# Kernel tuning notes

Measured on AMD Instinct MI355X. Metric: run time of the kernel, lower is better.

The kernel has to match this reference:

```python
import jax, jax.numpy as jnp
import numpy as np
import math

DIM = 896
NH = 8
HD = DIM // NH  # 112
B, T, KA_RAW, KT = 64, 8, 64, 512
KA = KA_RAW + 1  # adapter tokens + p conditioning token


def rope_cos_sin(L, hd):
    inv = 1.0 / (10000.0 ** (jnp.arange(0, hd, 2, dtype=jnp.float32) / hd))
    freqs = jnp.arange(L, dtype=jnp.float32)[:, None] * inv[None, :]  # (L, hd/2)
    emb = jnp.concatenate([freqs, freqs], axis=-1)  # (L, hd)
    return jnp.cos(emb), jnp.sin(emb)


def rotate_half(x):
    # interleaved rotation, faithful to the torch code
    x1 = x[..., ::2]
    x2 = x[..., 1::2]
    return jnp.stack((-x2, x1), axis=-1).reshape(x.shape)


def rope_apply(t, cos, sin):
    # cos/sin: (L, hd) broadcast over (B, H, L, hd)
    return t * cos + rotate_half(t) * sin


def heads(t):
    Bb, L, _ = t.shape
    return t.reshape(Bb, L, NH, HD).transpose(0, 2, 1, 3)  # (B, H, L, hd)


def setup_inputs() -> dict:
    key = jax.random.key(0)
    ks = jax.random.split(key, 32)
    s = 0.02
    d = {
        'x': jax.random.normal(ks[0], (B, T, DIM), jnp.float32),
        'h_a': jax.random.normal(ks[1], (B, KA_RAW, DIM), jnp.float32),
        'h_t': jax.random.normal(ks[2], (B, KT, DIM), jnp.float32),
        'p': jax.random.normal(ks[3], (B, 1, DIM), jnp.float32),
    }
    names = ['Wq', 'Wks', 'Wvs', 'Wka', 'Wva', 'Wkt', 'Wvt', 'Wo', 'Wf']
    for i, n in enumerate(names):
        d[n] = s * jax.random.normal(ks[4 + i], (DIM, DIM), jnp.float32)
        d['b' + n[1:]] = s * jax.random.normal(ks[16 + i], (DIM,), jnp.float32)
    d['gate'] = jnp.full((1,), 0.1, jnp.float32)  # nonzero so task branch is active
    d['ln_g'] = jnp.ones((DIM,), jnp.float32)
    d['ln_b'] = jnp.zeros((DIM,), jnp.float32)
    return d


def reference(x, h_a, h_t, p,
              Wq, bq, Wks, bks, Wvs, bvs, Wka, bka, Wva, bva,
              Wkt, bkt, Wvt, bvt, Wo, bo, Wf, bf,
              gate, ln_g, ln_b):
    ratio_g = jnp.tanh(gate)  # (1,)
    h_ad = jnp.concatenate([h_a, p], axis=1)  # (B, KA, C)

    q = heads(x @ Wq + bq)            # (B,H,T,hd)
    k_s = heads(x @ Wks + bks)
    v_s = heads(x @ Wvs + bvs)
    k_a = heads(h_ad @ Wka + bka)     # (B,H,KA,hd)
    v_a = heads(h_ad @ Wva + bva)
    k_t = heads(h_t @ Wkt + bkt)      # (B,H,KT,hd)
    v_t = heads(h_t @ Wvt + bvt)

    cos_m, sin_m = rope_cos_sin(T, HD)
    q = rope_apply(q, cos_m, sin_m)
    k_s = rope_apply(k_s, cos_m, sin_m)
    cos_a, sin_a = rope_cos_sin(KA, HD)
    k_a = rope_apply(k_a, cos_a, sin_a)
    cos_t, sin_t = rope_cos_sin(KT, HD)
    k_t = rope_apply(k_t, cos_t, sin_t)

    s_self = jnp.einsum('bhtd,bhkd->bhtk', q, k_s)
    s_ad = jnp.einsum('bhtd,bhkd->bhtk', q, k_a)
    s_task = jnp.einsum('bhtd,bhkd->bhtk', q, k_t) * ratio_g
    scores = jnp.concatenate([s_self, s_ad, s_task], axis=-1) / math.sqrt(HD)
    w = jax.nn.softmax(scores, axis=-1)  # (B,H,T,T+KA+KT)

    v = jnp.concatenate([v_s, v_a, v_t], axis=2)  # (B,H,T+KA+KT,hd)
    out = jnp.einsum('bhtk,bhkd->bhtd', w, v)
    out = out.transpose(0, 2, 1, 3).reshape(x.shape)  # (B,T,C)
    out = out @ Wo + bo

    y = out + x
    mu = jnp.mean(y, axis=-1, keepdims=True)
    var = jnp.var(y, axis=-1, keepdims=True)
    yn = (y - mu) / jnp.sqrt(var + 1e-5) * ln_g + ln_b
    return jax.nn.relu(yn @ Wf + bf)
```

## Files before the change

kernel.cpp:

```cpp
#include <hip/hip_runtime.h>
#include <hip/hip_bf16.h>
#include <math.h>

#define DIM 896
#define DD  (DIM * DIM)
#define NH 8
#define HD 112
#define BB 64
#define TT 8
#define KA 65
#define KAPAD 4224
#define KT 512
#define NKEYS (TT + KA + KT)
#define CH 4096

#define EPI_NONE  0
#define EPI_ROPE  1
#define EPI_RESID 2
#define EPI_RELU  3

#define NEG_L2_10K_OVER_56 (-0.2373327285062406f)

#ifndef __has_builtin
#define __has_builtin(x) 0
#endif
#if __has_builtin(__builtin_amdgcn_global_load_lds)
#define HAS_GLL 1
#else
#define HAS_GLL 0
#endif

typedef __attribute__((ext_vector_type(8))) short bf16x8_t;
typedef __attribute__((ext_vector_type(4))) float f32x4_t;

__device__ __forceinline__ short f2bf(float f) {
  unsigned u = __float_as_uint(f);
  u += 0x7fffu + ((u >> 16) & 1u);
  return (short)(u >> 16);
}
__device__ __forceinline__ float bf2f(short s) {
  return __uint_as_float(((unsigned)(unsigned short)s) << 16);
}

struct W9 { const float* w[9]; };

__global__ __launch_bounds__(256) void wtrans(W9 ws, short* __restrict__ Wt)
{
  __shared__ float t[32][33];
  const float* W = ws.w[blockIdx.z];
  short* dst = Wt + (size_t)blockIdx.z * DD;
  const int bx = blockIdx.x, by = blockIdx.y;
  const int tx = threadIdx.x & 31, ty = threadIdx.x >> 5;
#pragma unroll
  for (int i = 0; i < 4; ++i)
    t[ty + i * 8][tx] = W[(size_t)(by * 32 + ty + i * 8) * DIM + bx * 32 + tx];
  __syncthreads();
#pragma unroll
  for (int i = 0; i < 4; ++i)
    dst[(size_t)(bx * 32 + ty + i * 8) * DIM + by * 32 + tx] = f2bf(t[tx][ty + i * 8]);
}

__global__ __launch_bounds__(256) void convert_bf16(
    const float* __restrict__ src, short* __restrict__ dst, int n8)
{
  const int i = blockIdx.x * 256 + threadIdx.x;
  if (i >= n8) return;
  const float4 a = ((const float4*)src)[i * 2];
  const float4 b = ((const float4*)src)[i * 2 + 1];
  bf16x8_t o;
  o[0] = f2bf(a.x); o[1] = f2bf(a.y); o[2] = f2bf(a.z); o[3] = f2bf(a.w);
  o[4] = f2bf(b.x); o[5] = f2bf(b.y); o[6] = f2bf(b.z); o[7] = f2bf(b.w);
  ((bf16x8_t*)dst)[i] = o;
}

__global__ __launch_bounds__(256) void build_had(
    const float* __restrict__ h_a, const float* __restrict__ p,
    short* __restrict__ had)
{
  const int i = blockIdx.x * 256 + threadIdx.x;
  const int total = KAPAD * DIM / 8;
  if (i >= total) return;
  const int c = (i % 112) * 8;
  const int row = i / 112;
  bf16x8_t o;
  if (row >= BB * KA) {
#pragma unroll
    for (int j = 0; j < 8; ++j) o[j] = 0;
  } else {
    const int b = row / KA, j = row % KA;
    const float* src = (j < KA - 1) ? h_a + ((size_t)b * (KA - 1) + j) * DIM + c
                                    : p + (size_t)b * DIM + c;
    const float4 a = *(const float4*)src;
    const float4 d = *(const float4*)(src + 4);
    o[0] = f2bf(a.x); o[1] = f2bf(a.y); o[2] = f2bf(a.z); o[3] = f2bf(a.w);
    o[4] = f2bf(d.x); o[5] = f2bf(d.y); o[6] = f2bf(d.z); o[7] = f2bf(d.w);
  }
  ((bf16x8_t*)had)[i] = o;
}

struct EpiCfg {
  const float* bias[3];
  float* outF[3];
  short* outB[3];
  const float* resid;
  int epi[3];
  int pos_mod[3];
  int row_off;
  int hm[3];
  int hm_L[3];
  int hm_ltot[3];
};

__global__ __launch_bounds__(256) void gemm_bf16(
    const short* __restrict__ A, const short* __restrict__ Wt, EpiCfg cfg)
{
  __shared__ __align__(16) short As[128 * 32];
  __shared__ __align__(16) short Bs[128 * 32];
  const int tid = threadIdx.x;
  const int wave = tid >> 6, lane = tid & 63;
  const int sub = blockIdx.x / 7;
  const int col0 = (blockIdx.x % 7) * 128;
  const int row0 = blockIdx.y * 128;
  const int wm = wave >> 1, wn = wave & 1;
  const int lm = lane & 15, lq = lane >> 4;

  const int sm = lane >> 2, sk = (lane & 3) * 8;
  const short* Ag0 = A + (size_t)(row0 + wave * 32 + sm) * DIM + sk;
  const short* Ag1 = Ag0 + (size_t)16 * DIM;
  const short* Wg0 = Wt + (size_t)(sub * DIM + col0 + wave * 32 + sm) * DIM + sk;
  const short* Wg1 = Wg0 + (size_t)16 * DIM;

  f32x4_t acc[4][4];
#pragma unroll
  for (int i = 0; i < 4; ++i)
#pragma unroll
    for (int j = 0; j < 4; ++j) acc[i][j] = (f32x4_t){0.f, 0.f, 0.f, 0.f};

  for (int k0 = 0; k0 < DIM; k0 += 32) {
    __syncthreads();
#if HAS_GLL
    __builtin_amdgcn_global_load_lds(
        (const __attribute__((address_space(1))) unsigned*)(Ag0 + k0),
        (__attribute__((address_space(3))) unsigned*)&As[(wave * 32) * 32], 16, 0, 0);
    __builtin_amdgcn_global_load_lds(
        (const __attribute__((address_space(1))) unsigned*)(Ag1 + k0),
        (__attribute__((address_space(3))) unsigned*)&As[(wave * 32 + 16) * 32], 16, 0, 0);
    __builtin_amdgcn_global_load_lds(
        (const __attribute__((address_space(1))) unsigned*)(Wg0 + k0),
        (__attribute__((address_space(3))) unsigned*)&Bs[(wave * 32) * 32], 16, 0, 0);
    __builtin_amdgcn_global_load_lds(
        (const __attribute__((address_space(1))) unsigned*)(Wg1 + k0),
        (__attribute__((address_space(3))) unsigned*)&Bs[(wave * 32 + 16) * 32], 16, 0, 0);
#else
    {
      const int m = tid >> 1, kh = (tid & 1) * 16;
      *(bf16x8_t*)&As[m * 32 + kh] =
          *(const bf16x8_t*)(A + (size_t)(row0 + m) * DIM + k0 + kh);
      *(bf16x8_t*)&As[m * 32 + kh + 8] =
          *(const bf16x8_t*)(A + (size_t)(row0 + m) * DIM + k0 + kh + 8);
      *(bf16x8_t*)&Bs[m * 32 + kh] =
          *(const bf16x8_t*)(Wt + (size_t)(sub * DIM + col0 + m) * DIM + k0 + kh);
      *(bf16x8_t*)&Bs[m * 32 + kh + 8] =
          *(const bf16x8_t*)(Wt + (size_t)(sub * DIM + col0 + m) * DIM + k0 + kh + 8);
    }
#endif
    __syncthreads();

    bf16x8_t af[4], bfr[4];
#pragma unroll
    for (int t = 0; t < 4; ++t)
      af[t] = *(const bf16x8_t*)&As[(wm * 64 + t * 16 + lm) * 32 + lq * 8];
#pragma unroll
    for (int t = 0; t < 4; ++t)
      bfr[t] = *(const bf16x8_t*)&Bs[(wn * 64 + t * 16 + lm) * 32 + lq * 8];
#pragma unroll
    for (int tm = 0; tm < 4; ++tm)
#pragma unroll
      for (int tn = 0; tn < 4; ++tn)
        acc[tm][tn] = __builtin_amdgcn_mfma_f32_16x16x32_bf16(
            af[tm], bfr[tn], acc[tm][tn], 0, 0, 0);
  }

  const float* bias = cfg.bias[sub];
  float* outF = cfg.outF[sub];
  short* outB = cfg.outB[sub];
  const int epi = cfg.epi[sub], pm = cfg.pos_mod[sub];
  const int hm = cfg.hm[sub];
  const int L = cfg.hm_L[sub], ltot = cfg.hm_ltot[sub];
  int gb[4][4], gl[4][4];
  if (hm) {
#pragma unroll
    for (int tm = 0; tm < 4; ++tm) {
      const int g = cfg.row_off + row0 + wm * 64 + tm * 16 + lq * 4;
      int bq2 = g / L;
      int l = g - bq2 * L;
#pragma unroll
      for (int r = 0; r < 4; ++r) {
        gb[tm][r] = bq2; gl[tm][r] = l;
        if (++l == L) { l = 0; ++bq2; }
      }
    }
  }
#pragma unroll
  for (int tn = 0; tn < 4; ++tn) {
    const int col = col0 + wn * 64 + tn * 16 + lm;
    const float bv = bias[col];
    int hcol = 0, dcol = 0;
    if (hm) { hcol = col / HD; dcol = col - hcol * HD; }
    float fr = 0.f, sgn = 0.f;
    if (epi == EPI_ROPE) {
      const int d0 = col % HD;
      fr = exp2f((float)(d0 % 56) * NEG_L2_10K_OVER_56);
      sgn = (d0 & 1) ? 1.f : -1.f;
    }
#pragma unroll
    for (int tm = 0; tm < 4; ++tm) {
#pragma unroll
      for (int r = 0; r < 4; ++r) {
        const int grow = cfg.row_off + row0 + wm * 64 + tm * 16 + lq * 4 + r;
        float v = acc[tm][tn][r] + bv;
        if (epi == EPI_ROPE) {
          const float prt = __shfl_xor(v, 1);
          const int pos = hm ? gl[tm][r] : (grow % pm);
          float s, c;
          __sincosf((float)pos * fr, &s, &c);
          v = v * c + sgn * prt * s;
        } else if (epi == EPI_RESID) {
          v += cfg.resid[(size_t)grow * DIM + col];
        } else if (epi == EPI_RELU) {
          v = fmaxf(v, 0.f);
        }
        if (hm) {
          if (gb[tm][r] < BB)
            outB[((size_t)(gb[tm][r] * NH + hcol) * ltot + gl[tm][r]) * HD + dcol] =
                f2bf(v);
        } else if (outB) {
          outB[(size_t)grow * DIM + col] = f2bf(v);
        } else {
          outF[(size_t)grow * DIM + col] = v;
        }
      }
    }
  }
}

#define SCP 10

__global__ __launch_bounds__(1024, 8) void attn_kernel(
    const short* __restrict__ q, const short* __restrict__ kall,
    const short* __restrict__ vall, const float* __restrict__ gate,
    short* __restrict__ out)
{
  __shared__ __align__(16) float qs[TT * HD];
  __shared__ __align__(16) float sc[NKEYS * SCP];
  __shared__ float red[TT * TT * HD];
  __shared__ float isum[TT];
  const int tid = threadIdx.x;
  const int bh = blockIdx.x;
  const float scale = 0.09449111825230681f;
  const float rg = tanhf(gate[0]);

  if (tid < TT * HD) qs[tid] = bf2f(q[(size_t)bh * (TT * HD) + tid]);
  __syncthreads();

  if (tid < NKEYS) {
    const int k = tid;
    const short* kp = kall + ((size_t)bh * NKEYS + k) * HD;
    float dot[TT] = {};
    for (int d8 = 0; d8 < HD; d8 += 8) {
      const bf16x8_t kv8 = *(const bf16x8_t*)(kp + d8);
      float kf[8];
#pragma unroll
      for (int j = 0; j < 8; ++j) kf[j] = bf2f(kv8[j]);
#pragma unroll
      for (int t = 0; t < TT; ++t) {
        const float4 qa = *(const float4*)&qs[t * HD + d8];
        const float4 qb4 = *(const float4*)&qs[t * HD + d8 + 4];
        dot[t] = fmaf(qa.x, kf[0], dot[t]);
        dot[t] = fmaf(qa.y, kf[1], dot[t]);
        dot[t] = fmaf(qa.z, kf[2], dot[t]);
        dot[t] = fmaf(qa.w, kf[3], dot[t]);
        dot[t] = fmaf(qb4.x, kf[4], dot[t]);
        dot[t] = fmaf(qb4.y, kf[5], dot[t]);
        dot[t] = fmaf(qb4.z, kf[6], dot[t]);
        dot[t] = fmaf(qb4.w, kf[7], dot[t]);
      }
    }
    const float s = (k >= TT + KA) ? scale * rg : scale;
#pragma unroll
    for (int t = 0; t < TT; ++t) sc[k * SCP + t] = dot[t] * s;
  }
  __syncthreads();

  const int wave = tid >> 6, lane = tid & 63;
  if (wave < TT) {
    const int t = wave;
    float m = -1e30f;
    for (int k = lane; k < NKEYS; k += 64) m = fmaxf(m, sc[k * SCP + t]);
#pragma unroll
    for (int o = 32; o >= 1; o >>= 1) m = fmaxf(m, __shfl_xor(m, o));
    float sum = 0.f;
    for (int k = lane; k < NKEYS; k += 64) {
      const float e = expf(sc[k * SCP + t] - m);
      sc[k * SCP + t] = e;
      sum += e;
    }
#pragma unroll
    for (int o = 32; o >= 1; o >>= 1) sum += __shfl_xor(sum, o);
    if (lane == 0) isum[t] = 1.f / sum;
  }
  __syncthreads();

  if (tid < TT * HD) {
    const int g = tid / HD, d = tid - g * HD;
    const int kb = (g * NKEYS) / TT, ke = ((g + 1) * NKEYS) / TT;
    const short* vp = vall + (size_t)bh * (NKEYS * HD) + d;
    float acc[TT] = {};
    for (int k = kb; k < ke; ++k) {
      const float vv = bf2f(vp[(size_t)k * HD]);
      const float2 s0 = *(const float2*)&sc[k * SCP];
      const float2 s1 = *(const float2*)&sc[k * SCP + 2];
      const float2 s2 = *(const float2*)&sc[k * SCP + 4];
      const float2 s3 = *(const float2*)&sc[k * SCP + 6];
      acc[0] = fmaf(s0.x, vv, acc[0]);
      acc[1] = fmaf(s0.y, vv, acc[1]);
      acc[2] = fmaf(s1.x, vv, acc[2]);
      acc[3] = fmaf(s1.y, vv, acc[3]);
      acc[4] = fmaf(s2.x, vv, acc[4]);
      acc[5] = fmaf(s2.y, vv, acc[5]);
      acc[6] = fmaf(s3.x, vv, acc[6]);
      acc[7] = fmaf(s3.y, vv, acc[7]);
    }
#pragma unroll
    for (int t = 0; t < TT; ++t) red[(g * TT + t) * HD + d] = acc[t];
  }
  __syncthreads();

  if (tid < TT * HD) {
    const int t = tid / HD, d = tid - t * HD;
    float a = 0.f;
#pragma unroll
    for (int g = 0; g < TT; ++g) a += red[(g * TT + t) * HD + d];
    out[((size_t)(bh >> 3) * TT + t) * DIM + (bh & 7) * HD + d] = f2bf(a * isum[t]);
  }
}

__global__ __launch_bounds__(256) void ln_kernel(
    const float* __restrict__ y, const float* __restrict__ g,
    const float* __restrict__ beta, short* __restrict__ yn)
{
  __shared__ float s1[4], s2[4];
  const int r = blockIdx.x, tid = threadIdx.x;
  const float* row = y + (size_t)r * DIM;
  float sum = 0.f, sq = 0.f;
  for (int c = tid; c < DIM; c += 256) {
    const float v = row[c];
    sum += v;
    sq = fmaf(v, v, sq);
  }
#pragma unroll
  for (int o = 32; o >= 1; o >>= 1) {
    sum += __shfl_xor(sum, o);
    sq  += __shfl_xor(sq, o);
  }
  const int wave = tid >> 6, lane = tid & 63;
  if (lane == 0) { s1[wave] = sum; s2[wave] = sq; }
  __syncthreads();
  sum = s1[0] + s1[1] + s1[2] + s1[3];
  sq  = s2[0] + s2[1] + s2[2] + s2[3];
  const float mu = sum / DIM;
  const float var = sq / DIM - mu * mu;
  const float rstd = 1.f / sqrtf(var + 1e-5f);
  for (int c = tid; c < DIM; c += 256)
    yn[(size_t)r * DIM + c] = f2bf((row[c] - mu) * rstd * g[c] + beta[c]);
}

extern "C" void kernel_launch(void* const* d_in, const int* in_sizes, int n_in,
                              void* d_out, int out_size, void* d_ws, size_t ws_size,
                              hipStream_t stream)
{
  const float* x   = (const float*)d_in[0];
  const float* h_a = (const float*)d_in[1];
  const float* h_t = (const float*)d_in[2];
  const float* p   = (const float*)d_in[3];
  const float* Wq  = (const float*)d_in[4];  const float* bq  = (const float*)d_in[5];
  const float* Wks = (const float*)d_in[6];  const float* bks = (const float*)d_in[7];
  const float* Wvs = (const float*)d_in[8];  const float* bvs = (const float*)d_in[9];
  const float* Wka = (const float*)d_in[10]; const float* bka = (const float*)d_in[11];
  const float* Wva = (const float*)d_in[12]; const float* bva = (const float*)d_in[13];
  const float* Wkt = (const float*)d_in[14]; const float* bkt = (const float*)d_in[15];
  const float* Wvt = (const float*)d_in[16]; const float* bvt = (const float*)d_in[17];
  const float* Wo  = (const float*)d_in[18]; const float* bo  = (const float*)d_in[19];
  const float* Wf  = (const float*)d_in[20]; const float* bf_ = (const float*)d_in[21];
  const float* gate = (const float*)d_in[22];
  const float* ln_g = (const float*)d_in[23];
  const float* ln_b = (const float*)d_in[24];

  const size_t SZ_HAD = (size_t)KAPAD * DIM * 2;
  const size_t SZ_SM  = (size_t)BB * TT * DIM * 2;
  const size_t SZ_KV  = (size_t)BB * NH * NKEYS * HD * 2;
  const size_t SZ_WT  = (size_t)9 * DD * 2;
  const size_t needed = SZ_HAD + SZ_SM * 4 + SZ_KV * 2 + SZ_WT
                        + (size_t)BB * TT * DIM * 4;
  if (ws_size < needed) return;

  char* wsp = (char*)d_ws;
  short* hadb = (short*)wsp; wsp += SZ_HAD;
  short* xb   = (short*)wsp; wsp += SZ_SM;
  short* qb   = (short*)wsp; wsp += SZ_SM;
  short* kall = (short*)wsp; wsp += SZ_KV;
  short* vall = (short*)wsp; wsp += SZ_KV;
  short* WtA  = (short*)wsp; wsp += SZ_WT;
  short* attn_outb = (short*)wsp; wsp += SZ_SM;
  float* yb   = (float*)wsp; wsp += (size_t)BB * TT * DIM * 4;
  short* ynb  = (short*)wsp; wsp += SZ_SM;
  short* scratch = WtA;

  dim3 blk(256);

  W9 w9; const float* Ws[9] = {Wq, Wks, Wvs, Wka, Wva, Wkt, Wvt, Wo, Wf};
  for (int i = 0; i < 9; ++i) w9.w[i] = Ws[i];
  wtrans<<<dim3(28, 28, 9), blk, 0, stream>>>(w9, WtA);

  convert_bf16<<<(BB * TT * DIM / 8 + 255) / 256, blk, 0, stream>>>(x, xb, BB * TT * DIM / 8);
  build_had<<<(KAPAD * DIM / 8 + 255) / 256, blk, 0, stream>>>(h_a, p, hadb);

  {
    EpiCfg c = {};
    c.bias[0] = bq;  c.outB[0] = qb;   c.epi[0] = EPI_ROPE; c.pos_mod[0] = TT;
    c.hm[0] = 1; c.hm_L[0] = TT; c.hm_ltot[0] = TT;
    c.bias[1] = bks; c.outB[1] = kall; c.epi[1] = EPI_ROPE; c.pos_mod[1] = TT;
    c.hm[1] = 1; c.hm_L[1] = TT; c.hm_ltot[1] = NKEYS;
    c.bias[2] = bvs; c.outB[2] = vall; c.epi[2] = EPI_NONE; c.pos_mod[2] = 1;
    c.hm[2] = 1; c.hm_L[2] = TT; c.hm_ltot[2] = NKEYS;
    gemm_bf16<<<dim3(21, BB * TT / 128), blk, 0, stream>>>(xb, WtA, c);
  }
  {
    EpiCfg c = {};
    c.bias[0] = bka; c.outB[0] = kall + (size_t)TT * HD; c.epi[0] = EPI_ROPE;
    c.pos_mod[0] = KA; c.hm[0] = 1; c.hm_L[0] = KA; c.hm_ltot[0] = NKEYS;
    c.bias[1] = bva; c.outB[1] = vall + (size_t)TT * HD; c.epi[1] = EPI_NONE;
    c.pos_mod[1] = 1; c.hm[1] = 1; c.hm_L[1] = KA; c.hm_ltot[1] = NKEYS;
    gemm_bf16<<<dim3(14, KAPAD / 128), blk, 0, stream>>>(hadb, WtA + (size_t)3 * DD, c);
  }
  for (int m0 = 0; m0 < BB * KT; m0 += CH) {
    convert_bf16<<<(CH * DIM / 8 + 255) / 256, blk, 0, stream>>>(
        h_t + (size_t)m0 * DIM, scratch, CH * DIM / 8);
    EpiCfg c = {};
    c.bias[0] = bkt; c.outB[0] = kall + (size_t)(TT + KA) * HD; c.epi[0] = EPI_ROPE;
    c.pos_mod[0] = KT; c.hm[0] = 1; c.hm_L[0] = KT; c.hm_ltot[0] = NKEYS;
    c.bias[1] = bvt; c.outB[1] = vall + (size_t)(TT + KA) * HD; c.epi[1] = EPI_NONE;
    c.pos_mod[1] = 1; c.hm[1] = 1; c.hm_L[1] = KT; c.hm_ltot[1] = NKEYS;
    c.row_off = m0;
    gemm_bf16<<<dim3(14, CH / 128), blk, 0, stream>>>(scratch, WtA + (size_t)5 * DD, c);
  }

  attn_kernel<<<BB * NH, dim3(1024), 0, stream>>>(qb, kall, vall, gate, attn_outb);

  {
    EpiCfg c = {};
    c.bias[0] = bo; c.outF[0] = yb; c.epi[0] = EPI_RESID; c.pos_mod[0] = 1;
    c.resid = x;
    gemm_bf16<<<dim3(7, BB * TT / 128), blk, 0, stream>>>(attn_outb, WtA + (size_t)7 * DD, c);
  }
  ln_kernel<<<BB * TT, blk, 0, stream>>>(yb, ln_g, ln_b, ynb);
  {
    EpiCfg c = {};
    c.bias[0] = bf_; c.outF[0] = (float*)d_out; c.epi[0] = EPI_RELU; c.pos_mod[0] = 1;
    gemm_bf16<<<dim3(7, BB * TT / 128), blk, 0, stream>>>(ynb, WtA + (size_t)8 * DD, c);
  }
}
```

Baseline: 790.3 us.

## Tile K/V through shared memory in attention kernel with padded key layout

The attention kernel now stages K and V in shared-memory tiles of 148 keys, loaded with coalesced 16-byte reads, instead of having each thread stream its own key row or strided V column from global memory. The QK stage maps threads to (key, query) pairs, and the PV stage spreads keys across 16 lanes with shuffle reductions, which removes the red[] buffer and one barrier. The key dimension is padded to 592, which needs a zero_pad kernel and masked scores. This targets uncoalesced global loads and low thread utilisation, at the cost of extra barriers and an extra small launch.

Measured after the change: 1.047 ms. 32.5% more time.

```diff
diff --git a/kernel.cpp b/kernel.cpp
--- a/kernel.cpp
+++ b/kernel.cpp
@@ -12,6 +12,8 @@
 #define KAPAD 4224
 #define KT 512
 #define NKEYS (TT + KA + KT)
+#define NKP 592
+#define KTILE 148
 #define CH 4096
 
 #define EPI_NONE  0
@@ -96,6 +98,21 @@
     o[4] = f2bf(d.x); o[5] = f2bf(d.y); o[6] = f2bf(d.z); o[7] = f2bf(d.w);
   }
   ((bf16x8_t*)had)[i] = o;
+}
+
+__global__ __launch_bounds__(256) void zero_pad(short* __restrict__ vall)
+{
+  const int i = blockIdx.x * 256 + threadIdx.x;
+  const int PADR = NKP - NKEYS;
+  const int total = BB * NH * PADR * (HD / 8);
+  if (i >= total) return;
+  const int o = i % (HD / 8);
+  const int r = (i / (HD / 8)) % PADR;
+  const int bh = i / ((HD / 8) * PADR);
+  bf16x8_t z;
+#pragma unroll
+  for (int j = 0; j < 8; ++j) z[j] = 0;
+  ((bf16x8_t*)(vall + ((size_t)bh * NKP + NKEYS + r) * HD))[o] = z;
 }
 
 struct EpiCfg {
@@ -244,6 +261,7 @@
   }
 }
 
+#define QSP 116
 #define SCP 10
 
 __global__ __launch_bounds__(1024, 8) void attn_kernel(
@@ -251,44 +269,62 @@
     const short* __restrict__ vall, const float* __restrict__ gate,
     short* __restrict__ out)
 {
-  __shared__ __align__(16) float qs[TT * HD];
-  __shared__ __align__(16) float sc[NKEYS * SCP];
-  __shared__ float red[TT * TT * HD];
+  __shared__ __align__(16) float qs[TT * QSP];
+  __shared__ __align__(16) float sc[NKP * SCP];
+  __shared__ __align__(16) short kv[KTILE * HD];
   __shared__ float isum[TT];
   const int tid = threadIdx.x;
   const int bh = blockIdx.x;
   const float scale = 0.09449111825230681f;
   const float rg = tanhf(gate[0]);
-
-  if (tid < TT * HD) qs[tid] = bf2f(q[(size_t)bh * (TT * HD) + tid]);
-  __syncthreads();
-
-  if (tid < NKEYS) {
-    const int k = tid;
-    const short* kp = kall + ((size_t)bh * NKEYS + k) * HD;
-    float dot[TT] = {};
-    for (int d8 = 0; d8 < HD; d8 += 8) {
-      const bf16x8_t kv8 = *(const bf16x8_t*)(kp + d8);
-      float kf[8];
-#pragma unroll
-      for (int j = 0; j < 8; ++j) kf[j] = bf2f(kv8[j]);
-#pragma unroll
-      for (int t = 0; t < TT; ++t) {
-        const float4 qa = *(const float4*)&qs[t * HD + d8];
-        const float4 qb4 = *(const float4*)&qs[t * HD + d8 + 4];
-        dot[t] = fmaf(qa.x, kf[0], dot[t]);
-        dot[t] = fmaf(qa.y, kf[1], dot[t]);
-        dot[t] = fmaf(qa.z, kf[2], dot[t]);
-        dot[t] = fmaf(qa.w, kf[3], dot[t]);
-        dot[t] = fmaf(qb4.x, kf[4], dot[t]);
-        dot[t] = fmaf(qb4.y, kf[5], dot[t]);
-        dot[t] = fmaf(qb4.z, kf[6], dot[t]);
-        dot[t] = fmaf(qb4.w, kf[7], dot[t]);
+  const size_t kvbase = (size_t)bh * (NKP * HD);
+
+  if (tid < TT * HD) {
+    const int t = tid / HD, d = tid - t * HD;
+    qs[t * QSP + d] = bf2f(q[(size_t)bh * (TT * HD) + tid]);
+  }
+
+  for (int tile = 0; tile < 4; ++tile) {
+    const int base = tile * KTILE;
+    __syncthreads();
+    for (int i = tid; i < KTILE * HD / 8; i += 1024)
+      ((bf16x8_t*)kv)[i] =
+          *(const bf16x8_t*)(kall + kvbase + (size_t)base * HD + (size_t)i * 8);
+    __syncthreads();
+    for (int idx = tid; idx < KTILE * TT; idx += 1024) {
+      const int k = idx >> 3, t = idx & 7;
+      float d0 = 0.f, d1 = 0.f;
+#pragma unroll
+      for (int d8 = 0; d8 < HD; d8 += 16) {
+        const bf16x8_t ka8 = *(const bf16x8_t*)&kv[k * HD + d8];
+        const bf16x8_t kb8 = *(const bf16x8_t*)&kv[k * HD + d8 + 8];
+        const float4 qa = *(const float4*)&qs[t * QSP + d8];
+        const float4 qb4 = *(const float4*)&qs[t * QSP + d8 + 4];
+        const float4 qc = *(const float4*)&qs[t * QSP + d8 + 8];
+        const float4 qd = *(const float4*)&qs[t * QSP + d8 + 12];
+        d0 = fmaf(qa.x, bf2f(ka8[0]), d0);
+        d0 = fmaf(qa.y, bf2f(ka8[1]), d0);
+        d0 = fmaf(qa.z, bf2f(ka8[2]), d0);
+        d0 = fmaf(qa.w, bf2f(ka8[3]), d0);
+        d0 = fmaf(qb4.x, bf2f(ka8[4]), d0);
+        d0 = fmaf(qb4.y, bf2f(ka8[5]), d0);
+        d0 = fmaf(qb4.z, bf2f(ka8[6]), d0);
+        d0 = fmaf(qb4.w, bf2f(ka8[7]), d0);
+        d1 = fmaf(qc.x, bf2f(kb8[0]), d1);
+        d1 = fmaf(qc.y, bf2f(kb8[1]), d1);
+        d1 = fmaf(qc.z, bf2f(kb8[2]), d1);
+        d1 = fmaf(qc.w, bf2f(kb8[3]), d1);
+        d1 = fmaf(qd.x, bf2f(kb8[4]), d1);
+        d1 = fmaf(qd.y, bf2f(kb8[5]), d1);
+        d1 = fmaf(qd.z, bf2f(kb8[6]), d1);
+        d1 = fmaf(qd.w, bf2f(kb8[7]), d1);
       }
-    }
-    const float s = (k >= TT + KA) ? scale * rg : scale;
-#pragma unroll
-    for (int t = 0; t < TT; ++t) sc[k * SCP + t] = dot[t] * s;
+      const int key = base + k;
+      float v;
+      if (key >= NKEYS) v = -1e30f;
+      else v = (d0 + d1) * ((key >= TT + KA) ? scale * rg : scale);
+      sc[key * SCP + t] = v;
+    }
   }
   __syncthreads();
 
@@ -296,11 +332,11 @@
   if (wave < TT) {
     const int t = wave;
     float m = -1e30f;
-    for (int k = lane; k < NKEYS; k += 64) m = fmaxf(m, sc[k * SCP + t]);
+    for (int k = lane; k < NKP; k += 64) m = fmaxf(m, sc[k * SCP + t]);
 #pragma unroll
     for (int o = 32; o >= 1; o >>= 1) m = fmaxf(m, __shfl_xor(m, o));
     float sum = 0.f;
-    for (int k = lane; k < NKEYS; k += 64) {
+    for (int k = lane; k < NKP; k += 64) {
       const float e = expf(sc[k * SCP + t] - m);
       sc[k * SCP + t] = e;
       sum += e;
@@ -309,39 +345,51 @@
     for (int o = 32; o >= 1; o >>= 1) sum += __shfl_xor(sum, o);
     if (lane == 0) isum[t] = 1.f / sum;
   }
-  __syncthreads();
-
-  if (tid < TT * HD) {
-    const int g = tid / HD, d = tid - g * HD;
-    const int kb = (g * NKEYS) / TT, ke = ((g + 1) * NKEYS) / TT;
-    const short* vp = vall + (size_t)bh * (NKEYS * HD) + d;
-    float acc[TT] = {};
-    for (int k = kb; k < ke; ++k) {
-      const float vv = bf2f(vp[(size_t)k * HD]);
-      const float2 s0 = *(const float2*)&sc[k * SCP];
-      const float2 s1 = *(const float2*)&sc[k * SCP + 2];
-      const float2 s2 = *(const float2*)&sc[k * SCP + 4];
-      const float2 s3 = *(const float2*)&sc[k * SCP + 6];
-      acc[0] = fmaf(s0.x, vv, acc[0]);
-      acc[1] = fmaf(s0.y, vv, acc[1]);
-      acc[2] = fmaf(s1.x, vv, acc[2]);
-      acc[3] = fmaf(s1.y, vv, acc[3]);
-      acc[4] = fmaf(s2.x, vv, acc[4]);
-      acc[5] = fmaf(s2.y, vv, acc[5]);
-      acc[6] = fmaf(s3.x, vv, acc[6]);
-      acc[7] = fmaf(s3.y, vv, acc[7]);
-    }
-#pragma unroll
-    for (int t = 0; t < TT; ++t) red[(g * TT + t) * HD + d] = acc[t];
-  }
-  __syncthreads();
-
-  if (tid < TT * HD) {
-    const int t = tid / HD, d = tid - t * HD;
-    float a = 0.f;
-#pragma unroll
-    for (int g = 0; g < TT; ++g) a += red[(g * TT + t) * HD + d];
-    out[((size_t)(bh >> 3) * TT + t) * DIM + (bh & 7) * HD + d] = f2bf(a * isum[t]);
+
+  const int kg = tid & 15, dp = tid >> 4;
+  float acc[16] = {};
+  for (int tile = 0; tile < 4; ++tile) {
+    const int base = tile * KTILE;
+    __syncthreads();
+    for (int i = tid; i < KTILE * HD / 8; i += 1024)
+      ((bf16x8_t*)kv)[i] =
+          *(const bf16x8_t*)(vall + kvbase + (size_t)base * HD + (size_t)i * 8);
+    __syncthreads();
+    if (dp < 56) {
+      for (int k = kg; k < KTILE; k += 16) {
+        const unsigned v2 = *(const unsigned*)&kv[k * HD + dp * 2];
+        const float vlo = __uint_as_float(v2 << 16);
+        const float vhi = __uint_as_float(v2 & 0xffff0000u);
+        const float* sp = &sc[(base + k) * SCP];
+        const float2 s0 = *(const float2*)(sp);
+        const float2 s1 = *(const float2*)(sp + 2);
+        const float2 s2 = *(const float2*)(sp + 4);
+        const float2 s3 = *(const float2*)(sp + 6);
+        acc[0]  = fmaf(s0.x, vlo, acc[0]);  acc[1]  = fmaf(s0.x, vhi, acc[1]);
+        acc[2]  = fmaf(s0.y, vlo, acc[2]);  acc[3]  = fmaf(s0.y, vhi, acc[3]);
+        acc[4]  = fmaf(s1.x, vlo, acc[4]);  acc[5]  = fmaf(s1.x, vhi, acc[5]);
+        acc[6]  = fmaf(s1.y, vlo, acc[6]);  acc[7]  = fmaf(s1.y, vhi, acc[7]);
+        acc[8]  = fmaf(s2.x, vlo, acc[8]);  acc[9]  = fmaf(s2.x, vhi, acc[9]);
+        acc[10] = fmaf(s2.y, vlo, acc[10]); acc[11] = fmaf(s2.y, vhi, acc[11]);
+        acc[12] = fmaf(s3.x, vlo, acc[12]); acc[13] = fmaf(s3.x, vhi, acc[13]);
+        acc[14] = fmaf(s3.y, vlo, acc[14]); acc[15] = fmaf(s3.y, vhi, acc[15]);
+      }
+    }
+  }
+  if (dp < 56) {
+#pragma unroll
+    for (int a = 0; a < 16; ++a) {
+      float v = acc[a];
+      v += __shfl_xor(v, 1);
+      v += __shfl_xor(v, 2);
+      v += __shfl_xor(v, 4);
+      v += __shfl_xor(v, 8);
+      acc[a] = v;
+    }
+    const int t = kg >> 1, dd = kg & 1;
+    const int d = dp * 2 + dd;
+    const float o = acc[t * 2 + dd] * isum[t];
+    out[((size_t)(bh >> 3) * TT + t) * DIM + (bh & 7) * HD + d] = f2bf(o);
   }
 }
 
@@ -398,7 +446,7 @@
 
   const size_t SZ_HAD = (size_t)KAPAD * DIM * 2;
   const size_t SZ_SM  = (size_t)BB * TT * DIM * 2;
-  const size_t SZ_KV  = (size_t)BB * NH * NKEYS * HD * 2;
+  const size_t SZ_KV  = (size_t)BB * NH * NKP * HD * 2;
   const size_t SZ_WT  = (size_t)9 * DD * 2;
   const size_t needed = SZ_HAD + SZ_SM * 4 + SZ_KV * 2 + SZ_WT
                         + (size_t)BB * TT * DIM * 4;
@@ -424,23 +472,24 @@
 
   convert_bf16<<<(BB * TT * DIM / 8 + 255) / 256, blk, 0, stream>>>(x, xb, BB * TT * DIM / 8);
   build_had<<<(KAPAD * DIM / 8 + 255) / 256, blk, 0, stream>>>(h_a, p, hadb);
+  zero_pad<<<(BB * NH * (NKP - NKEYS) * (HD / 8) + 255) / 256, blk, 0, stream>>>(vall);
 
   {
     EpiCfg c = {};
     c.bias[0] = bq;  c.outB[0] = qb;   c.epi[0] = EPI_ROPE; c.pos_mod[0] = TT;
     c.hm[0] = 1; c.hm_L[0] = TT; c.hm_ltot[0] = TT;
     c.bias[1] = bks; c.outB[1] = kall; c.epi[1] = EPI_ROPE; c.pos_mod[1] = TT;
-    c.hm[1] = 1; c.hm_L[1] = TT; c.hm_ltot[1] = NKEYS;
+    c.hm[1] = 1; c.hm_L[1] = TT; c.hm_ltot[1] = NKP;
     c.bias[2] = bvs; c.outB[2] = vall; c.epi[2] = EPI_NONE; c.pos_mod[2] = 1;
-    c.hm[2] = 1; c.hm_L[2] = TT; c.hm_ltot[2] = NKEYS;
+    c.hm[2] = 1; c.hm_L[2] = TT; c.hm_ltot[2] = NKP;
     gemm_bf16<<<dim3(21, BB * TT / 128), blk, 0, stream>>>(xb, WtA, c);
   }
   {
     EpiCfg c = {};
     c.bias[0] = bka; c.outB[0] = kall + (size_t)TT * HD; c.epi[0] = EPI_ROPE;
-    c.pos_mod[0] = KA; c.hm[0] = 1; c.hm_L[0] = KA; c.hm_ltot[0] = NKEYS;
+    c.pos_mod[0] = KA; c.hm[0] = 1; c.hm_L[0] = KA; c.hm_ltot[0] = NKP;
     c.bias[1] = bva; c.outB[1] = vall + (size_t)TT * HD; c.epi[1] = EPI_NONE;
-    c.pos_mod[1] = 1; c.hm[1] = 1; c.hm_L[1] = KA; c.hm_ltot[1] = NKEYS;
+    c.pos_mod[1] = 1; c.hm[1] = 1; c.hm_L[1] = KA; c.hm_ltot[1] = NKP;
     gemm_bf16<<<dim3(14, KAPAD / 128), blk, 0, stream>>>(hadb, WtA + (size_t)3 * DD, c);
   }
   for (int m0 = 0; m0 < BB * KT; m0 += CH) {
@@ -448,9 +497,9 @@
         h_t + (size_t)m0 * DIM, scratch, CH * DIM / 8);
     EpiCfg c = {};
     c.bias[0] = bkt; c.outB[0] = kall + (size_t)(TT + KA) * HD; c.epi[0] = EPI_ROPE;
-    c.pos_mod[0] = KT; c.hm[0] = 1; c.hm_L[0] = KT; c.hm_ltot[0] = NKEYS;
+    c.pos_mod[0] = KT; c.hm[0] = 1; c.hm_L[0] = KT; c.hm_ltot[0] = NKP;
     c.bias[1] = bvt; c.outB[1] = vall + (size_t)(TT + KA) * HD; c.epi[1] = EPI_NONE;
-    c.pos_mod[1] = 1; c.hm[1] = 1; c.hm_L[1] = KT; c.hm_ltot[1] = NKEYS;
+    c.pos_mod[1] = 1; c.hm[1] = 1; c.hm_L[1] = KT; c.hm_ltot[1] = NKP;
     c.row_off = m0;
     gemm_bf16<<<dim3(14, CH / 128), blk, 0, stream>>>(scratch, WtA + (size_t)5 * DD, c);
   }
```

## Fuse fp32-to-bf16 conversion of activations into GEMM A-tile loads

Applied to the files above, without the earlier changes.

Removes the separate convert_bf16 passes for x and h_t; the GEMM now reads fp32 activations directly and converts them to bf16 while staging the A tile in LDS. This also removes the chunked loop over h_t, so the K/V-task GEMM runs as one full-size launch. The cost is that A-tile loads become synchronous register loads plus conversion instead of asynchronous global_load_lds, and each A element is read as fp32 (twice the bytes) once per column block.

Result: slower. 920.5 us (+16.5%).

```diff
diff --git a/kernel.cpp b/kernel.cpp
--- a/kernel.cpp
+++ b/kernel.cpp
@@ -12,7 +12,6 @@
 #define KAPAD 4224
 #define KT 512
 #define NKEYS (TT + KA + KT)
-#define CH 4096
 
 #define EPI_NONE  0
 #define EPI_ROPE  1
@@ -58,19 +57,6 @@
 #pragma unroll
   for (int i = 0; i < 4; ++i)
     dst[(size_t)(bx * 32 + ty + i * 8) * DIM + by * 32 + tx] = f2bf(t[tx][ty + i * 8]);
-}
-
-__global__ __launch_bounds__(256) void convert_bf16(
-    const float* __restrict__ src, short* __restrict__ dst, int n8)
-{
-  const int i = blockIdx.x * 256 + threadIdx.x;
-  if (i >= n8) return;
-  const float4 a = ((const float4*)src)[i * 2];
-  const float4 b = ((const float4*)src)[i * 2 + 1];
-  bf16x8_t o;
-  o[0] = f2bf(a.x); o[1] = f2bf(a.y); o[2] = f2bf(a.z); o[3] = f2bf(a.w);
-  o[4] = f2bf(b.x); o[5] = f2bf(b.y); o[6] = f2bf(b.z); o[7] = f2bf(b.w);
-  ((bf16x8_t*)dst)[i] = o;
 }
 
 __global__ __launch_bounds__(256) void build_had(
@@ -111,8 +97,10 @@
   int hm_ltot[3];
 };
 
+template <bool AF32>
 __global__ __launch_bounds__(256) void gemm_bf16(
-    const short* __restrict__ A, const short* __restrict__ Wt, EpiCfg cfg)
+    const short* __restrict__ A, const float* __restrict__ Af,
+    const short* __restrict__ Wt, EpiCfg cfg)
 {
   __shared__ __align__(16) short As[128 * 32];
   __shared__ __align__(16) short Bs[128 * 32];
@@ -138,13 +126,28 @@
 
   for (int k0 = 0; k0 < DIM; k0 += 32) {
     __syncthreads();
+    if constexpr (AF32) {
+#pragma unroll
+      for (int c = tid; c < 512; c += 256) {
+        const int m = c >> 2, ko = (c & 3) * 8;
+        const float* srcp = Af + (size_t)(row0 + m) * DIM + k0 + ko;
+        const float4 a0 = *(const float4*)srcp;
+        const float4 a1 = *(const float4*)(srcp + 4);
+        bf16x8_t o;
+        o[0] = f2bf(a0.x); o[1] = f2bf(a0.y); o[2] = f2bf(a0.z); o[3] = f2bf(a0.w);
+        o[4] = f2bf(a1.x); o[5] = f2bf(a1.y); o[6] = f2bf(a1.z); o[7] = f2bf(a1.w);
+        *(bf16x8_t*)&As[c * 8] = o;
+      }
+    }
 #if HAS_GLL
-    __builtin_amdgcn_global_load_lds(
-        (const __attribute__((address_space(1))) unsigned*)(Ag0 + k0),
-        (__attribute__((address_space(3))) unsigned*)&As[(wave * 32) * 32], 16, 0, 0);
-    __builtin_amdgcn_global_load_lds(
-        (const __attribute__((address_space(1))) unsigned*)(Ag1 + k0),
-        (__attribute__((address_space(3))) unsigned*)&As[(wave * 32 + 16) * 32], 16, 0, 0);
+    if constexpr (!AF32) {
+      __builtin_amdgcn_global_load_lds(
+          (const __attribute__((address_space(1))) unsigned*)(Ag0 + k0),
+          (__attribute__((address_space(3))) unsigned*)&As[(wave * 32) * 32], 16, 0, 0);
+      __builtin_amdgcn_global_load_lds(
+          (const __attribute__((address_space(1))) unsigned*)(Ag1 + k0),
+          (__attribute__((address_space(3))) unsigned*)&As[(wave * 32 + 16) * 32], 16, 0, 0);
+    }
     __builtin_amdgcn_global_load_lds(
         (const __attribute__((address_space(1))) unsigned*)(Wg0 + k0),
         (__attribute__((address_space(3))) unsigned*)&Bs[(wave * 32) * 32], 16, 0, 0);
@@ -154,10 +157,12 @@
 #else
     {
       const int m = tid >> 1, kh = (tid & 1) * 16;
-      *(bf16x8_t*)&As[m * 32 + kh] =
-          *(const bf16x8_t*)(A + (size_t)(row0 + m) * DIM + k0 + kh);
-      *(bf16x8_t*)&As[m * 32 + kh + 8] =
-          *(const bf16x8_t*)(A + (size_t)(row0 + m) * DIM + k0 + kh + 8);
+      if constexpr (!AF32) {
+        *(bf16x8_t*)&As[m * 32 + kh] =
+            *(const bf16x8_t*)(A + (size_t)(row0 + m) * DIM + k0 + kh);
+        *(bf16x8_t*)&As[m * 32 + kh + 8] =
+            *(const bf16x8_t*)(A + (size_t)(row0 + m) * DIM + k0 + kh + 8);
+      }
       *(bf16x8_t*)&Bs[m * 32 + kh] =
           *(const bf16x8_t*)(Wt + (size_t)(sub * DIM + col0 + m) * DIM + k0 + kh);
       *(bf16x8_t*)&Bs[m * 32 + kh + 8] =
@@ -312,7 +317,7 @@
   __syncthreads();
 
   if (tid < TT * HD) {
-    const int g = tid / HD, d = tid - g * HD;
+    const int g = tid / HD, d = tid - (tid / HD) * HD;
     const int kb = (g * NKEYS) / TT, ke = ((g + 1) * NKEYS) / TT;
     const short* vp = vall + (size_t)bh * (NKEYS * HD) + d;
     float acc[TT] = {};
@@ -337,7 +342,7 @@
   __syncthreads();
 
   if (tid < TT * HD) {
-    const int t = tid / HD, d = tid - t * HD;
+    const int t = tid / HD, d = tid - (tid / HD) * HD;
     float a = 0.f;
 #pragma unroll
     for (int g = 0; g < TT; ++g) a += red[(g * TT + t) * HD + d];
@@ -400,13 +405,12 @@
   const size_t SZ_SM  = (size_t)BB * TT * DIM * 2;
   const size_t SZ_KV  = (size_t)BB * NH * NKEYS * HD * 2;
   const size_t SZ_WT  = (size_t)9 * DD * 2;
-  const size_t needed = SZ_HAD + SZ_SM * 4 + SZ_KV * 2 + SZ_WT
+  const size_t needed = SZ_HAD + SZ_SM * 3 + SZ_KV * 2 + SZ_WT
                         + (size_t)BB * TT * DIM * 4;
   if (ws_size < needed) return;
 
   char* wsp = (char*)d_ws;
   short* hadb = (short*)wsp; wsp += SZ_HAD;
-  short* xb   = (short*)wsp; wsp += SZ_SM;
   short* qb   = (short*)wsp; wsp += SZ_SM;
   short* kall = (short*)wsp; wsp += SZ_KV;
   short* vall = (short*)wsp; wsp += SZ_KV;
@@ -414,7 +418,6 @@
   short* attn_outb = (short*)wsp; wsp += SZ_SM;
   float* yb   = (float*)wsp; wsp += (size_t)BB * TT * DIM * 4;
   short* ynb  = (short*)wsp; wsp += SZ_SM;
-  short* scratch = WtA;
 
   dim3 blk(256);
 
@@ -422,7 +425,6 @@
   for (int i = 0; i < 9; ++i) w9.w[i] = Ws[i];
   wtrans<<<dim3(28, 28, 9), blk, 0, stream>>>(w9, WtA);
 
-  convert_bf16<<<(BB * TT * DIM / 8 + 255) / 256, blk, 0, stream>>>(x, xb, BB * TT * DIM / 8);
   build_had<<<(KAPAD * DIM / 8 + 255) / 256, blk, 0, stream>>>(h_a, p, hadb);
 
   {
@@ -433,7 +435,7 @@
     c.hm[1] = 1; c.hm_L[1] = TT; c.hm_ltot[1] = NKEYS;
     c.bias[2] = bvs; c.outB[2] = vall; c.epi[2] = EPI_NONE; c.pos_mod[2] = 1;
     c.hm[2] = 1; c.hm_L[2] = TT; c.hm_ltot[2] = NKEYS;
-    gemm_bf16<<<dim3(21, BB * TT / 128), blk, 0, stream>>>(xb, WtA, c);
+    gemm_bf16<true><<<dim3(21, BB * TT / 128), blk, 0, stream>>>(nullptr, x, WtA, c);
   }
   {
     EpiCfg c = {};
@@ -441,18 +443,18 @@
     c.pos_mod[0] = KA; c.hm[0] = 1; c.hm_L[0] = KA; c.hm_ltot[0] = NKEYS;
     c.bias[1] = bva; c.outB[1] = vall + (size_t)TT * HD; c.epi[1] = EPI_NONE;
     c.pos_mod[1] = 1; c.hm[1] = 1; c.hm_L[1] = KA; c.hm_ltot[1] = NKEYS;
-    gemm_bf16<<<dim3(14, KAPAD / 128), blk, 0, stream>>>(hadb, WtA + (size_t)3 * DD, c);
-  }
-  for (int m0 = 0; m0 < BB * KT; m0 += CH) {
-    convert_bf16<<<(CH * DIM / 8 + 255) / 256, blk, 0, stream>>>(
-        h_t + (size_t)m0 * DIM, scratch, CH * DIM / 8);
+    gemm_bf16<false><<<dim3(14, KAPAD / 128), blk, 0, stream>>>(
+        hadb, nullptr, WtA + (size_t)3 * DD, c);
+  }
+  {
     EpiCfg c = {};
     c.bias[0] = bkt; c.outB[0] = kall + (size_t)(TT + KA) * HD; c.epi[0] = EPI_ROPE;
     c.pos_mod[0] = KT; c.hm[0] = 1; c.hm_L[0] = KT; c.hm_ltot[0] = NKEYS;
     c.bias[1] = bvt; c.outB[1] = vall + (size_t)(TT + KA) * HD; c.epi[1] = EPI_NONE;
     c.pos_mod[1] = 1; c.hm[1] = 1; c.hm_L[1] = KT; c.hm_ltot[1] = NKEYS;
-    c.row_off = m0;
-    gemm_bf16<<<dim3(14, CH / 128), blk, 0, stream>>>(scratch, WtA + (size_t)5 * DD, c);
+    c.row_off = 0;
+    gemm_bf16<true><<<dim3(14, BB * KT / 128), blk, 0, stream>>>(
+        nullptr, h_t, WtA + (size_t)5 * DD, c);
   }
 
   attn_kernel<<<BB * NH, dim3(1024), 0, stream>>>(qb, kall, vall, gate, attn_outb);
@@ -461,12 +463,14 @@
     EpiCfg c = {};
     c.bias[0] = bo; c.outF[0] = yb; c.epi[0] = EPI_RESID; c.pos_mod[0] = 1;
     c.resid = x;
-    gemm_bf16<<<dim3(7, BB * TT / 128), blk, 0, stream>>>(attn_outb, WtA + (size_t)7 * DD, c);
+    gemm_bf16<false><<<dim3(7, BB * TT / 128), blk, 0, stream>>>(
+        attn_outb, nullptr, WtA + (size_t)7 * DD, c);
   }
   ln_kernel<<<BB * TT, blk, 0, stream>>>(yb, ln_g, ln_b, ynb);
   {
     EpiCfg c = {};
     c.bias[0] = bf_; c.outF[0] = (float*)d_out; c.epi[0] = EPI_RELU; c.pos_mod[0] = 1;
-    gemm_bf16<<<dim3(7, BB * TT / 128), blk, 0, stream>>>(ynb, WtA + (size_t)8 * DD, c);
-  }
-}
+    gemm_bf16<false><<<dim3(7, BB * TT / 128), blk, 0, stream>>>(
+        ynb, nullptr, WtA + (size_t)8 * DD, c);
+  }
+}
```
